# Kernel optimization log

Measured on AMD Instinct MI355X. Metric: run time of the kernel, lower is better.

## Reference

```python
import jax, jax.numpy as jnp
import numpy as np

EPS = 1e-06

def setup_inputs() -> dict:
    key = jax.random.key(0)
    kq, kk, kv = jax.random.split(key, 3)
    shape = (8, 16, 4096, 64)  # [B, H, N, D]
    q = jax.random.normal(kq, shape, dtype=jnp.float32)
    k = jax.random.normal(kk, shape, dtype=jnp.float32)
    v = jax.random.normal(kv, shape, dtype=jnp.float32)
    return {"q": q, "k": k, "v": v}

def reference(q, k, v):
    # softmax over sequence axis (n) for keys, over feature axis (d) for queries
    k_sm = jax.nn.softmax(k, axis=-2)   # [B,H,N,D]
    q_sm = jax.nn.softmax(q, axis=-1)   # [B,H,N,D]
    # context: [B,H,D,E] -- avoids the NxN attention matrix
    context = jnp.einsum('bhnd,bhne->bhde', k_sm, v)
    denom = jnp.sum(k_sm, axis=-2)[..., :, None] + EPS  # [B,H,D,1]
    context = context / denom
    out = jnp.einsum('bhnd,bhde->bhne', q_sm, context)  # [B,H,N,E]
    # dropout p=0.0 / eval mode -> identity
    return out
```

## Files before the change

### kernel.cpp

```cpp
#include <hip/hip_runtime.h>
#include <cstddef>
#include <cstdint>

#define BHN 128
#define NSEQ 4096
#define EPSF 1e-6f

constexpr int K2_S = 8;
constexpr int K2_ROWS = NSEQ / K2_S;
constexpr int K2_TILE = 64;
constexpr int K2_TILES = K2_ROWS / K2_TILE;

__global__ __launch_bounds__(256, 4)
void k2_partial_ctx(const float* __restrict__ K, const float* __restrict__ V,
                    float* __restrict__ part_ctx, float* __restrict__ part_cs)
{
    __shared__ __align__(16) float ke[K2_TILE * 64];
    __shared__ __align__(16) float vs[K2_TILE * 64];

    const int bh  = blockIdx.x;
    const int s   = blockIdx.y;
    const int tid = threadIdx.x;
    const int w    = tid >> 6;
    const int lane = tid & 63;
    const int l8   = lane & 7;
    const int h8   = lane >> 3;

    const float4* Kg = (const float4*)(K + ((size_t)bh * NSEQ + (size_t)s * K2_ROWS) * 64);
    const float4* Vg = (const float4*)(V + ((size_t)bh * NSEQ + (size_t)s * K2_ROWS) * 64);

    float acc[8][8];
    #pragma unroll
    for (int i = 0; i < 8; ++i)
        #pragma unroll
        for (int j = 0; j < 8; ++j) acc[i][j] = 0.f;
    float cs[8];
    #pragma unroll
    for (int i = 0; i < 8; ++i) cs[i] = 0.f;

    for (int t = 0; t < K2_TILES; ++t) {
        const float4* kt = Kg + t * (K2_TILE * 16);
        const float4* vt = Vg + t * (K2_TILE * 16);
        float4* ke4 = (float4*)ke;
        float4* vs4 = (float4*)vs;
        #pragma unroll
        for (int p = 0; p < 4; ++p) {
            const int f = tid + p * 256;
            float4 kq = kt[f];
            kq.x = __expf(kq.x);
            kq.y = __expf(kq.y);
            kq.z = __expf(kq.z);
            kq.w = __expf(kq.w);
            ke4[f] = kq;
            vs4[f] = vt[f];
        }
        __syncthreads();
        const float4* keR = (const float4*)ke;
        const float4* vsR = (const float4*)vs;
        #pragma unroll
        for (int nn = 0; nn < 16; ++nn) {
            const int n = w * 16 + nn;
            float4 a0 = keR[n * 16 + h8];
            float4 a1 = keR[n * 16 + 8 + h8];
            float4 b0 = vsR[n * 16 + l8];
            float4 b1 = vsR[n * 16 + 8 + l8];
            float a[8] = {a0.x, a0.y, a0.z, a0.w, a1.x, a1.y, a1.z, a1.w};
            float b[8] = {b0.x, b0.y, b0.z, b0.w, b1.x, b1.y, b1.z, b1.w};
            #pragma unroll
            for (int i = 0; i < 8; ++i) cs[i] += a[i];
            #pragma unroll
            for (int i = 0; i < 8; ++i)
                #pragma unroll
                for (int j = 0; j < 8; ++j)
                    acc[i][j] = fmaf(a[i], b[j], acc[i][j]);
        }
        __syncthreads();
    }

    float* red   = vs;
    float* redcs = ke;
    for (int wv = 0; wv < 4; ++wv) {
        if (w == wv) {
            #pragma unroll
            for (int i = 0; i < 8; ++i) {
                const int d = (i < 4) ? (4 * h8 + i) : (32 + 4 * h8 + (i - 4));
                #pragma unroll
                for (int ej = 0; ej < 2; ++ej) {
                    float4* dst = (float4*)&red[d * 64 + ej * 32 + 4 * l8];
                    float4 vv = make_float4(acc[i][4*ej+0], acc[i][4*ej+1],
                                            acc[i][4*ej+2], acc[i][4*ej+3]);
                    if (wv == 0) {
                        *dst = vv;
                    } else {
                        float4 o = *dst;
                        o.x += vv.x; o.y += vv.y; o.z += vv.z; o.w += vv.w;
                        *dst = o;
                    }
                }
                if (l8 == 0) {
                    if (wv == 0) redcs[d] = cs[i];
                    else         redcs[d] += cs[i];
                }
            }
        }
        __syncthreads();
    }

    float4* pc = (float4*)(part_ctx + (size_t)(bh * K2_S + s) * 4096);
    const float4* red4 = (const float4*)red;
    #pragma unroll
    for (int p = 0; p < 4; ++p) {
        const int f = tid + p * 256;
        pc[f] = red4[f];
    }
    if (tid < 16) {
        ((float4*)(part_cs + (size_t)(bh * K2_S + s) * 64))[tid] =
            ((const float4*)redcs)[tid];
    }
}

__global__ __launch_bounds__(256)
void k2_reduce(const float* __restrict__ part_ctx, const float* __restrict__ part_cs,
               float* __restrict__ ctxf)
{
    __shared__ float inv_cs[64];
    const int bh  = blockIdx.x;
    const int tid = threadIdx.x;
    if (tid < 64) {
        float c = 0.f;
        #pragma unroll
        for (int s = 0; s < K2_S; ++s)
            c += part_cs[(size_t)(bh * K2_S + s) * 64 + tid];
        inv_cs[tid] = 1.0f / (c * (1.0f + EPSF));
    }
    __syncthreads();
    const float4* pc = (const float4*)(part_ctx + (size_t)bh * K2_S * 4096);
    float4* cf = (float4*)(ctxf + (size_t)bh * 4096);
    const int f = blockIdx.y * 256 + tid;
    float4 sum = make_float4(0.f, 0.f, 0.f, 0.f);
    #pragma unroll
    for (int s = 0; s < K2_S; ++s) {
        float4 x = pc[s * 1024 + f];
        sum.x += x.x; sum.y += x.y; sum.z += x.z; sum.w += x.w;
    }
    const float inv = inv_cs[f >> 4];
    sum.x *= inv; sum.y *= inv; sum.z *= inv; sum.w *= inv;
    cf[f] = sum;
}

constexpr int K3_ROWS  = 128;
constexpr int QSTRIDE  = 66;

__global__ __launch_bounds__(128, 2)
void k3_out(const float* __restrict__ Q, const float* __restrict__ ctxf,
            float* __restrict__ out)
{
    __shared__ __align__(16) float qe[K3_ROWS * QSTRIDE];
    __shared__ __align__(16) float ctx_s[4096];
    __shared__ float rs[K3_ROWS];

    const int bh  = blockIdx.x;
    const int n0  = blockIdx.y * K3_ROWS;
    const int tid = threadIdx.x;
    const int w    = tid >> 6;
    const int lane = tid & 63;
    const int l8   = lane & 7;
    const int h8   = lane >> 3;

    {
        const float4* cg = (const float4*)(ctxf + (size_t)bh * 4096);
        float4* cs4 = (float4*)ctx_s;
        #pragma unroll
        for (int p = 0; p < 8; ++p)
            cs4[tid + p * 128] = cg[tid + p * 128];
    }
    {
        const float4* qg = (const float4*)(Q + ((size_t)bh * NSEQ + n0) * 64);
        const int rgrp = tid >> 4;
        const int c4   = tid & 15;
        for (int p = 0; p < 16; ++p) {
            const int rr = p * 8 + rgrp;
            float4 x = qg[rr * 16 + c4];
            x.x = __expf(x.x); x.y = __expf(x.y);
            x.z = __expf(x.z); x.w = __expf(x.w);
            float ssum = x.x + x.y + x.z + x.w;
            ssum += __shfl_xor(ssum, 1);
            ssum += __shfl_xor(ssum, 2);
            ssum += __shfl_xor(ssum, 4);
            ssum += __shfl_xor(ssum, 8);
            if (c4 == 0) rs[rr] = ssum;
            float* dst = qe + rr * QSTRIDE + 4 * c4;
            ((float2*)dst)[0] = make_float2(x.x, x.y);
            ((float2*)dst)[1] = make_float2(x.z, x.w);
        }
    }
    __syncthreads();

    int rowi[8];
    #pragma unroll
    for (int i = 0; i < 8; ++i)
        rowi[i] = 64 * w + ((i < 4) ? (4 * h8 + i) : (32 + 4 * h8 + (i - 4)));

    float acc[8][8];
    #pragma unroll
    for (int i = 0; i < 8; ++i)
        #pragma unroll
        for (int j = 0; j < 8; ++j) acc[i][j] = 0.f;

    for (int dc = 0; dc < 64; dc += 2) {
        float2 aq[8];
        #pragma unroll
        for (int i = 0; i < 8; ++i)
            aq[i] = *(const float2*)(qe + rowi[i] * QSTRIDE + dc);
        float4 b00 = *(const float4*)(ctx_s + dc * 64 + 4 * l8);
        float4 b01 = *(const float4*)(ctx_s + dc * 64 + 32 + 4 * l8);
        float4 b10 = *(const float4*)(ctx_s + (dc + 1) * 64 + 4 * l8);
        float4 b11 = *(const float4*)(ctx_s + (dc + 1) * 64 + 32 + 4 * l8);
        float b0[8] = {b00.x,b00.y,b00.z,b00.w,b01.x,b01.y,b01.z,b01.w};
        float b1[8] = {b10.x,b10.y,b10.z,b10.w,b11.x,b11.y,b11.z,b11.w};
        #pragma unroll
        for (int i = 0; i < 8; ++i) {
            #pragma unroll
            for (int j = 0; j < 8; ++j) {
                acc[i][j] = fmaf(aq[i].x, b0[j], acc[i][j]);
                acc[i][j] = fmaf(aq[i].y, b1[j], acc[i][j]);
            }
        }
    }

    float4* og = (float4*)(out + ((size_t)bh * NSEQ + n0) * 64);
    #pragma unroll
    for (int i = 0; i < 8; ++i) {
        const float inv = 1.0f / rs[rowi[i]];
        #pragma unroll
        for (int ej = 0; ej < 2; ++ej) {
            float4 vv = make_float4(acc[i][4*ej+0]*inv, acc[i][4*ej+1]*inv,
                                    acc[i][4*ej+2]*inv, acc[i][4*ej+3]*inv);
            og[rowi[i] * 16 + ej * 8 + l8] = vv;
        }
    }
}

extern "C" void kernel_launch(void* const* d_in, const int* in_sizes, int n_in,
                              void* d_out, int out_size, void* d_ws, size_t ws_size,
                              hipStream_t stream)
{
    const float* q = (const float*)d_in[0];
    const float* k = (const float*)d_in[1];
    const float* v = (const float*)d_in[2];
    float* out = (float*)d_out;

    float* part_ctx = (float*)d_out;
    float* part_cs  = (float*)d_ws;
    float* ctxf     = part_cs + (size_t)1024 * 64;

    k2_partial_ctx<<<dim3(BHN, K2_S), 256, 0, stream>>>(k, v, part_ctx, part_cs);
    k2_reduce<<<dim3(BHN, 4), 256, 0, stream>>>(part_ctx, part_cs, ctxf);
    k3_out<<<dim3(BHN, NSEQ / K3_ROWS), 128, 0, stream>>>(q, ctxf, out);
}
```

Measured before the change: 495.3 us.

## Prefetch K/V tiles into registers, tree-reduce partials, split Q load in halves

In the partial-context kernel, the next K/V tile is loaded into registers while the current tile is computed, which hides global latency, and one barrier per tile is dropped. The serial four-step wave reduction becomes a two-level tree reduction with a per-wave column-sum buffer. The output kernel moves to 256 threads and 256 rows per block, loads Q in two 32-column halves through a narrower padded LDS tile, and prefetches the second half while the first half is computed. The cost is more registers and extra barriers, which may reduce occupancy.

After: 1.949 ms. 293% more time.

```diff
diff --git a/kernel.cpp b/kernel.cpp
--- a/kernel.cpp
+++ b/kernel.cpp
@@ -8,15 +8,19 @@
 
 constexpr int K2_S = 8;
 constexpr int K2_ROWS = NSEQ / K2_S;
-constexpr int K2_TILE = 64;
-constexpr int K2_TILES = K2_ROWS / K2_TILE;
+constexpr int K2_TILES = 8;
+
+__device__ __forceinline__ float4 exp4(float4 x) {
+    return make_float4(__expf(x.x), __expf(x.y), __expf(x.z), __expf(x.w));
+}
 
 __global__ __launch_bounds__(256, 4)
 void k2_partial_ctx(const float* __restrict__ K, const float* __restrict__ V,
                     float* __restrict__ part_ctx, float* __restrict__ part_cs)
 {
-    __shared__ __align__(16) float ke[K2_TILE * 64];
-    __shared__ __align__(16) float vs[K2_TILE * 64];
+    __shared__ __align__(16) float ke[64 * 64];
+    __shared__ __align__(16) float vs[64 * 64];
+    __shared__ float csb[256];
 
     const int bh  = blockIdx.x;
     const int s   = blockIdx.y;
@@ -38,32 +42,38 @@
     #pragma unroll
     for (int i = 0; i < 8; ++i) cs[i] = 0.f;
 
+    float4* ke4 = (float4*)ke;
+    float4* vs4 = (float4*)vs;
+
+    float4 kreg[4], vreg[4];
+    #pragma unroll
+    for (int p = 0; p < 4; ++p) {
+        kreg[p] = Kg[tid + p * 256];
+        vreg[p] = Vg[tid + p * 256];
+    }
+
     for (int t = 0; t < K2_TILES; ++t) {
-        const float4* kt = Kg + t * (K2_TILE * 16);
-        const float4* vt = Vg + t * (K2_TILE * 16);
-        float4* ke4 = (float4*)ke;
-        float4* vs4 = (float4*)vs;
+        if (t) __syncthreads();
         #pragma unroll
         for (int p = 0; p < 4; ++p) {
-            const int f = tid + p * 256;
-            float4 kq = kt[f];
-            kq.x = __expf(kq.x);
-            kq.y = __expf(kq.y);
-            kq.z = __expf(kq.z);
-            kq.w = __expf(kq.w);
-            ke4[f] = kq;
-            vs4[f] = vt[f];
+            ke4[tid + p * 256] = exp4(kreg[p]);
+            vs4[tid + p * 256] = vreg[p];
+        }
+        if (t + 1 < K2_TILES) {
+            #pragma unroll
+            for (int p = 0; p < 4; ++p) {
+                kreg[p] = Kg[(t + 1) * 1024 + tid + p * 256];
+                vreg[p] = Vg[(t + 1) * 1024 + tid + p * 256];
+            }
         }
         __syncthreads();
-        const float4* keR = (const float4*)ke;
-        const float4* vsR = (const float4*)vs;
         #pragma unroll
         for (int nn = 0; nn < 16; ++nn) {
             const int n = w * 16 + nn;
-            float4 a0 = keR[n * 16 + h8];
-            float4 a1 = keR[n * 16 + 8 + h8];
-            float4 b0 = vsR[n * 16 + l8];
-            float4 b1 = vsR[n * 16 + 8 + l8];
+            float4 a0 = ke4[n * 16 + h8];
+            float4 a1 = ke4[n * 16 + 8 + h8];
+            float4 b0 = vs4[n * 16 + l8];
+            float4 b1 = vs4[n * 16 + 8 + l8];
             float a[8] = {a0.x, a0.y, a0.z, a0.w, a1.x, a1.y, a1.z, a1.w};
             float b[8] = {b0.x, b0.y, b0.z, b0.w, b1.x, b1.y, b1.z, b1.w};
             #pragma unroll
@@ -74,49 +84,75 @@
                 for (int j = 0; j < 8; ++j)
                     acc[i][j] = fmaf(a[i], b[j], acc[i][j]);
         }
-        __syncthreads();
-    }
-
-    float* red   = vs;
-    float* redcs = ke;
-    for (int wv = 0; wv < 4; ++wv) {
-        if (w == wv) {
-            #pragma unroll
-            for (int i = 0; i < 8; ++i) {
-                const int d = (i < 4) ? (4 * h8 + i) : (32 + 4 * h8 + (i - 4));
-                #pragma unroll
-                for (int ej = 0; ej < 2; ++ej) {
-                    float4* dst = (float4*)&red[d * 64 + ej * 32 + 4 * l8];
-                    float4 vv = make_float4(acc[i][4*ej+0], acc[i][4*ej+1],
-                                            acc[i][4*ej+2], acc[i][4*ej+3]);
-                    if (wv == 0) {
-                        *dst = vv;
-                    } else {
-                        float4 o = *dst;
-                        o.x += vv.x; o.y += vv.y; o.z += vv.z; o.w += vv.w;
-                        *dst = o;
-                    }
-                }
-                if (l8 == 0) {
-                    if (wv == 0) redcs[d] = cs[i];
-                    else         redcs[d] += cs[i];
-                }
+    }
+    __syncthreads();
+
+    int dd[8];
+    #pragma unroll
+    for (int i = 0; i < 8; ++i)
+        dd[i] = (i < 4) ? (4 * h8 + i) : (32 + 4 * h8 + (i - 4));
+
+    if (l8 == 0) {
+        #pragma unroll
+        for (int i = 0; i < 8; ++i) csb[w * 64 + dd[i]] = cs[i];
+    }
+    if (w >= 2) {
+        float* dst = (w == 2) ? ke : vs;
+        #pragma unroll
+        for (int i = 0; i < 8; ++i)
+            #pragma unroll
+            for (int ej = 0; ej < 2; ++ej)
+                *(float4*)&dst[dd[i] * 64 + ej * 32 + 4 * l8] =
+                    make_float4(acc[i][4*ej+0], acc[i][4*ej+1],
+                                acc[i][4*ej+2], acc[i][4*ej+3]);
+    }
+    __syncthreads();
+    if (w < 2) {
+        const float* src = (w == 0) ? ke : vs;
+        #pragma unroll
+        for (int i = 0; i < 8; ++i)
+            #pragma unroll
+            for (int ej = 0; ej < 2; ++ej) {
+                float4 o = *(const float4*)&src[dd[i] * 64 + ej * 32 + 4 * l8];
+                acc[i][4*ej+0] += o.x; acc[i][4*ej+1] += o.y;
+                acc[i][4*ej+2] += o.z; acc[i][4*ej+3] += o.w;
+            }
+    }
+    __syncthreads();
+    if (w == 1) {
+        #pragma unroll
+        for (int i = 0; i < 8; ++i)
+            #pragma unroll
+            for (int ej = 0; ej < 2; ++ej)
+                *(float4*)&ke[dd[i] * 64 + ej * 32 + 4 * l8] =
+                    make_float4(acc[i][4*ej+0], acc[i][4*ej+1],
+                                acc[i][4*ej+2], acc[i][4*ej+3]);
+    }
+    __syncthreads();
+    if (w == 0) {
+        #pragma unroll
+        for (int i = 0; i < 8; ++i) {
+            #pragma unroll
+            for (int ej = 0; ej < 2; ++ej) {
+                float4 o = *(const float4*)&ke[dd[i] * 64 + ej * 32 + 4 * l8];
+                *(float4*)&vs[dd[i] * 64 + ej * 32 + 4 * l8] =
+                    make_float4(acc[i][4*ej+0] + o.x, acc[i][4*ej+1] + o.y,
+                                acc[i][4*ej+2] + o.z, acc[i][4*ej+3] + o.w);
+            }
+            if (l8 == 0) {
+                float c = csb[dd[i]] + csb[64 + dd[i]] + csb[128 + dd[i]] + csb[192 + dd[i]];
+                csb[dd[i]] = c;
             }
         }
-        __syncthreads();
-    }
+    }
+    __syncthreads();
 
     float4* pc = (float4*)(part_ctx + (size_t)(bh * K2_S + s) * 4096);
-    const float4* red4 = (const float4*)red;
-    #pragma unroll
-    for (int p = 0; p < 4; ++p) {
-        const int f = tid + p * 256;
-        pc[f] = red4[f];
-    }
-    if (tid < 16) {
-        ((float4*)(part_cs + (size_t)(bh * K2_S + s) * 64))[tid] =
-            ((const float4*)redcs)[tid];
-    }
+    #pragma unroll
+    for (int p = 0; p < 4; ++p)
+        pc[tid + p * 256] = vs4[tid + p * 256];
+    if (tid < 16)
+        ((float4*)(part_cs + (size_t)(bh * K2_S + s) * 64))[tid] = ((const float4*)csb)[tid];
 }
 
 __global__ __launch_bounds__(256)
@@ -148,52 +184,54 @@
     cf[f] = sum;
 }
 
-constexpr int K3_ROWS  = 128;
-constexpr int QSTRIDE  = 66;
-
-__global__ __launch_bounds__(128, 2)
+constexpr int K3R = 256;
+constexpr int QST = 34;
+
+__global__ __launch_bounds__(256, 3)
 void k3_out(const float* __restrict__ Q, const float* __restrict__ ctxf,
             float* __restrict__ out)
 {
-    __shared__ __align__(16) float qe[K3_ROWS * QSTRIDE];
+    __shared__ __align__(16) float qe[K3R * QST];
     __shared__ __align__(16) float ctx_s[4096];
-    __shared__ float rs[K3_ROWS];
+    __shared__ float rs[K3R];
 
     const int bh  = blockIdx.x;
-    const int n0  = blockIdx.y * K3_ROWS;
+    const int n0  = blockIdx.y * K3R;
     const int tid = threadIdx.x;
     const int w    = tid >> 6;
     const int lane = tid & 63;
     const int l8   = lane & 7;
     const int h8   = lane >> 3;
-
-    {
-        const float4* cg = (const float4*)(ctxf + (size_t)bh * 4096);
-        float4* cs4 = (float4*)ctx_s;
-        #pragma unroll
-        for (int p = 0; p < 8; ++p)
-            cs4[tid + p * 128] = cg[tid + p * 128];
-    }
-    {
-        const float4* qg = (const float4*)(Q + ((size_t)bh * NSEQ + n0) * 64);
-        const int rgrp = tid >> 4;
-        const int c4   = tid & 15;
-        for (int p = 0; p < 16; ++p) {
-            const int rr = p * 8 + rgrp;
-            float4 x = qg[rr * 16 + c4];
-            x.x = __expf(x.x); x.y = __expf(x.y);
-            x.z = __expf(x.z); x.w = __expf(x.w);
-            float ssum = x.x + x.y + x.z + x.w;
-            ssum += __shfl_xor(ssum, 1);
-            ssum += __shfl_xor(ssum, 2);
-            ssum += __shfl_xor(ssum, 4);
-            ssum += __shfl_xor(ssum, 8);
-            if (c4 == 0) rs[rr] = ssum;
-            float* dst = qe + rr * QSTRIDE + 4 * c4;
-            ((float2*)dst)[0] = make_float2(x.x, x.y);
-            ((float2*)dst)[1] = make_float2(x.z, x.w);
-        }
-    }
+    const int rq   = tid >> 3;
+    const int c8   = tid & 7;
+
+    const float4* Qg = (const float4*)(Q + ((size_t)bh * NSEQ + n0) * 64);
+    const float4* Cg = (const float4*)(ctxf + (size_t)bh * 4096);
+
+    float4 creg[4];
+    #pragma unroll
+    for (int p = 0; p < 4; ++p) creg[p] = Cg[tid + p * 256];
+    float4 qreg[8];
+    #pragma unroll
+    for (int p = 0; p < 8; ++p) qreg[p] = Qg[(rq + 32 * p) * 16 + c8];
+
+    float4* cs4 = (float4*)ctx_s;
+    #pragma unroll
+    for (int p = 0; p < 4; ++p) cs4[tid + p * 256] = creg[p];
+
+    #pragma unroll
+    for (int p = 0; p < 8; ++p) {
+        const int r = rq + 32 * p;
+        float4 e = exp4(qreg[p]);
+        float ssum = e.x + e.y + e.z + e.w;
+        ssum += __shfl_xor(ssum, 1);
+        ssum += __shfl_xor(ssum, 2);
+        ssum += __shfl_xor(ssum, 4);
+        if (c8 == 0) rs[r] = ssum;
+        *(float4*)&qe[r * QST + 4 * c8] = e;
+    }
+    #pragma unroll
+    for (int p = 0; p < 8; ++p) qreg[p] = Qg[(rq + 32 * p) * 16 + 8 + c8];
     __syncthreads();
 
     int rowi[8];
@@ -207,11 +245,12 @@
         #pragma unroll
         for (int j = 0; j < 8; ++j) acc[i][j] = 0.f;
 
-    for (int dc = 0; dc < 64; dc += 2) {
+    #pragma unroll
+    for (int dc = 0; dc < 32; dc += 2) {
         float2 aq[8];
         #pragma unroll
         for (int i = 0; i < 8; ++i)
-            aq[i] = *(const float2*)(qe + rowi[i] * QSTRIDE + dc);
+            aq[i] = *(const float2*)(qe + rowi[i] * QST + dc);
         float4 b00 = *(const float4*)(ctx_s + dc * 64 + 4 * l8);
         float4 b01 = *(const float4*)(ctx_s + dc * 64 + 32 + 4 * l8);
         float4 b10 = *(const float4*)(ctx_s + (dc + 1) * 64 + 4 * l8);
@@ -219,13 +258,47 @@
         float b0[8] = {b00.x,b00.y,b00.z,b00.w,b01.x,b01.y,b01.z,b01.w};
         float b1[8] = {b10.x,b10.y,b10.z,b10.w,b11.x,b11.y,b11.z,b11.w};
         #pragma unroll
-        for (int i = 0; i < 8; ++i) {
+        for (int i = 0; i < 8; ++i)
             #pragma unroll
             for (int j = 0; j < 8; ++j) {
                 acc[i][j] = fmaf(aq[i].x, b0[j], acc[i][j]);
                 acc[i][j] = fmaf(aq[i].y, b1[j], acc[i][j]);
             }
-        }
+    }
+    __syncthreads();
+
+    #pragma unroll
+    for (int p = 0; p < 8; ++p) {
+        const int r = rq + 32 * p;
+        float4 e = exp4(qreg[p]);
+        float ssum = e.x + e.y + e.z + e.w;
+        ssum += __shfl_xor(ssum, 1);
+        ssum += __shfl_xor(ssum, 2);
+        ssum += __shfl_xor(ssum, 4);
+        if (c8 == 0) rs[r] += ssum;
+        *(float4*)&qe[r * QST + 4 * c8] = e;
+    }
+    __syncthreads();
+
+    #pragma unroll
+    for (int dc = 0; dc < 32; dc += 2) {
+        float2 aq[8];
+        #pragma unroll
+        for (int i = 0; i < 8; ++i)
+            aq[i] = *(const float2*)(qe + rowi[i] * QST + dc);
+        float4 b00 = *(const float4*)(ctx_s + (32 + dc) * 64 + 4 * l8);
+        float4 b01 = *(const float4*)(ctx_s + (32 + dc) * 64 + 32 + 4 * l8);
+        float4 b10 = *(const float4*)(ctx_s + (33 + dc) * 64 + 4 * l8);
+        float4 b11 = *(const float4*)(ctx_s + (33 + dc) * 64 + 32 + 4 * l8);
+        float b0[8] = {b00.x,b00.y,b00.z,b00.w,b01.x,b01.y,b01.z,b01.w};
+        float b1[8] = {b10.x,b10.y,b10.z,b10.w,b11.x,b11.y,b11.z,b11.w};
+        #pragma unroll
+        for (int i = 0; i < 8; ++i)
+            #pragma unroll
+            for (int j = 0; j < 8; ++j) {
+                acc[i][j] = fmaf(aq[i].x, b0[j], acc[i][j]);
+                acc[i][j] = fmaf(aq[i].y, b1[j], acc[i][j]);
+            }
     }
 
     float4* og = (float4*)(out + ((size_t)bh * NSEQ + n0) * 64);
@@ -233,11 +306,10 @@
     for (int i = 0; i < 8; ++i) {
         const float inv = 1.0f / rs[rowi[i]];
         #pragma unroll
-        for (int ej = 0; ej < 2; ++ej) {
-            float4 vv = make_float4(acc[i][4*ej+0]*inv, acc[i][4*ej+1]*inv,
-                                    acc[i][4*ej+2]*inv, acc[i][4*ej+3]*inv);
-            og[rowi[i] * 16 + ej * 8 + l8] = vv;
-        }
+        for (int ej = 0; ej < 2; ++ej)
+            og[rowi[i] * 16 + ej * 8 + l8] =
+                make_float4(acc[i][4*ej+0]*inv, acc[i][4*ej+1]*inv,
+                            acc[i][4*ej+2]*inv, acc[i][4*ej+3]*inv);
     }
 }
 
@@ -256,5 +328,5 @@
 
     k2_partial_ctx<<<dim3(BHN, K2_S), 256, 0, stream>>>(k, v, part_ctx, part_cs);
     k2_reduce<<<dim3(BHN, 4), 256, 0, stream>>>(part_ctx, part_cs, ctxf);
-    k3_out<<<dim3(BHN, NSEQ / K3_ROWS), 128, 0, stream>>>(q, ctxf, out);
-}
+    k3_out<<<dim3(BHN, NSEQ / K3R), 256, 0, stream>>>(q, ctxf, out);
+}
```
